# Kernel tuning notes

Hardware: AMD Instinct MI355X
Metric: run time of the kernel (lower is better)

## Reference

```python
import jax, jax.numpy as jnp
import numpy as np

B, CIN, H, W = 8, 128, 64, 64
COUT, KH, KW = 128, 3, 3
STRIDE = (1, 1)
PAD = (1, 1)
DIL = (1, 1)
GROUPS = 1
OFFSET_GROUPS = 1

def _out_size(i, k, s, p, d):
    return (i + 2 * p - d * (k - 1) - 1) // s + 1

HO = _out_size(H, KH, STRIDE[0], PAD[0], DIL[0])
WO = _out_size(W, KW, STRIDE[1], PAD[1], DIL[1])


def setup_inputs() -> dict:
    key = jax.random.key(0)
    k1, k2, k3, k4 = jax.random.split(key, 4)
    x = jax.random.normal(k1, (B, CIN, H, W), jnp.float32)
    offset = jax.random.normal(k2, (B, 2 * OFFSET_GROUPS * KH * KW, HO, WO), jnp.float32)
    fan_in = (CIN // GROUPS) * KH * KW
    bound = 1.0 / np.sqrt(fan_in)
    weight = jax.random.uniform(k3, (COUT, CIN // GROUPS, KH, KW), jnp.float32, -bound, bound)
    bias = jax.random.uniform(k4, (COUT,), jnp.float32, -bound, bound)
    return {"x": x, "offset": offset, "weight": weight, "bias": bias}


def _deform_conv2d(x, offset, weight, bias):
    Bn, Cin, Hi, Wi = x.shape
    K = KH * KW
    Goff, Gw = OFFSET_GROUPS, GROUPS
    Cpg = Cin // Goff

    # base sampling positions (before learned offsets)
    ys = jnp.arange(HO, dtype=jnp.float32) * STRIDE[0] - PAD[0]  # [HO]
    xs = jnp.arange(WO, dtype=jnp.float32) * STRIDE[1] - PAD[1]  # [WO]
    base_y = jnp.repeat(jnp.arange(KH, dtype=jnp.float32) * DIL[0], KW)  # [K]
    base_x = jnp.tile(jnp.arange(KW, dtype=jnp.float32) * DIL[1], KH)    # [K]

    # offsets: channel layout is 2*(g*K + k) + {0: dy, 1: dx}
    off = offset.reshape(Bn, Goff, K, 2, HO, WO)
    py = base_y[None, None, :, None, None] + ys[None, None, None, :, None] + off[:, :, :, 0]  # [B,Goff,K,HO,WO]
    px = base_x[None, None, :, None, None] + xs[None, None, None, None, :] + off[:, :, :, 1]

    y0 = jnp.floor(py)
    x0 = jnp.floor(px)
    ly = py - y0  # fractional weights
    lx = px - x0

    xg = x.reshape(Bn, Goff, Cpg, Hi * Wi)

    def gather_one(img, lin):  # img [Cpg, H*W], lin [K,HO,WO] -> [Cpg,K,HO,WO]
        return img[:, lin]

    gather = jax.vmap(jax.vmap(gather_one))  # over B and Goff

    def corner(yi, xi, w):
        # zero-padding semantics: out-of-bounds corner contributes 0
        mask = (yi >= 0) & (yi < Hi) & (xi >= 0) & (xi < Wi)
        iy = jnp.clip(yi, 0, Hi - 1).astype(jnp.int32)
        ix = jnp.clip(xi, 0, Wi - 1).astype(jnp.int32)
        lin = iy * Wi + ix  # [B,Goff,K,HO,WO]
        wm = (w * mask.astype(x.dtype))[:, :, None]  # broadcast over channel axis
        return gather(xg, lin) * wm  # [B,Goff,Cpg,K,HO,WO]

    val = (corner(y0, x0, (1 - ly) * (1 - lx))
           + corner(y0, x0 + 1, (1 - ly) * lx)
           + corner(y0 + 1, x0, ly * (1 - lx))
           + corner(y0 + 1, x0 + 1, ly * lx))  # [B,Goff,Cpg,K,HO,WO]

    # grouped conv accumulate
    val = val.reshape(Bn, Gw, Cin // Gw, K, HO, WO)
    wg = weight.reshape(Gw, COUT // Gw, Cin // Gw, K)
    out = jnp.einsum('bgckhw,gock->bgohw', val, wg).reshape(Bn, COUT, HO, WO)
    return out + bias[None, :, None, None]


def reference(x, offset, weight, bias):
    return _deform_conv2d(x, offset, weight, bias)
```

## Files before the change

kernel.cpp:

```cpp
#include <hip/hip_runtime.h>

typedef unsigned int   u32;
typedef unsigned short u16;
typedef short bf16x8 __attribute__((ext_vector_type(8)));
typedef float f32x4  __attribute__((ext_vector_type(4)));

#define CIN   128
#define COUT  128
#define Hh    64
#define Ww    64
#define Bb    8
#define KPOS  9
#define KDIM  (CIN*KPOS)
#define NKSTEP 36
#define XT_ELEMS (Bb*Hh*Ww*CIN)

__device__ __forceinline__ float bflo(u32 u){ return __uint_as_float(u << 16); }
__device__ __forceinline__ float bfhi(u32 u){ return __uint_as_float(u & 0xffff0000u); }

__device__ __forceinline__ u32 packbf(float a, float b){
    u32 ua = __float_as_uint(a);
    u32 ub = __float_as_uint(b);
    ua += 0x7fffu + ((ua >> 16) & 1u);
    ub += 0x7fffu + ((ub >> 16) & 1u);
    return (ua >> 16) | (ub & 0xffff0000u);
}
__device__ __forceinline__ u16 tobf(float a){
    u32 ua = __float_as_uint(a);
    ua += 0x7fffu + ((ua >> 16) & 1u);
    return (u16)(ua >> 16);
}

__global__ __launch_bounds__(256) void k_transpose(const float* __restrict__ x,
                                                   u16* __restrict__ xT){
    __shared__ float tile[32*33];
    int bi = blockIdx.x;
    int st = bi & 127, ct = (bi >> 7) & 3, b = bi >> 9;
    int sb = st * 32, cb = ct * 32;
    int tid = threadIdx.x;

    int i = tid >> 5, j = tid & 31;
    const float* xp = x + ((size_t)(b*CIN + cb) * 4096) + sb;
#pragma unroll
    for (int rr = 0; rr < 4; ++rr){
        int ci = i + rr*8;
        tile[ci*33 + j] = xp[(size_t)ci*4096 + j];
    }
    __syncthreads();

    int ii = tid >> 4, jj = tid & 15;
    u32* outp = (u32*)xT + ((size_t)b*4096 + sb)*64 + (cb >> 1) + jj;
#pragma unroll
    for (int rr = 0; rr < 2; ++rr){
        int sl = ii + rr*16;
        float v0 = tile[(2*jj  )*33 + sl];
        float v1 = tile[(2*jj+1)*33 + sl];
        outp[(size_t)sl*64] = packbf(v0, v1);
    }
}

__global__ __launch_bounds__(256) void k_wprep(const float* __restrict__ w,
                                               u16* __restrict__ Wt){
    int gid = blockIdx.x*256 + threadIdx.x;
    int jf   = gid & 7;
    int lane = (gid >> 3) & 63;
    int mt   = (gid >> 9) & 7;
    int kt   = gid >> 12;
    int m  = mt*16 + (lane & 15);
    int kk = (lane >> 4)*8 + jf;
    int ck = kt*32 + kk;
    int kpos = ck >> 7;
    int cin  = ck & 127;
    Wt[gid] = tobf(w[((size_t)m*128 + cin)*9 + kpos]);
}

__global__ __launch_bounds__(256, 2)
void k_main(const float* __restrict__ off, const float* __restrict__ bias,
            const u16* __restrict__ xT, const u16* __restrict__ Wt,
            float* __restrict__ out){
    __shared__ u32 Vsm[2][64*20];

    int tid = threadIdx.x;
    int bi  = blockIdx.x;
    int b   = bi & 7;
    int t   = bi >> 3;
    int s0  = t * 64;

    int p  = tid >> 2, qt = tid & 3;
    int ho = t;
    int wo = p;
    const u16* xb_base = xT + (size_t)b * (Hh*Ww*CIN);

    int lane = tid & 63, wave = tid >> 6;
    int wm = wave >> 1, wn = wave & 1;
    int quad = lane >> 4, l16 = lane & 15;

    f32x4 acc[4][2];
#pragma unroll
    for (int i = 0; i < 4; ++i)
#pragma unroll
        for (int j = 0; j < 2; ++j) acc[i][j] = {0.f, 0.f, 0.f, 0.f};

    int   aa[4];
    float wt[4];

    auto state = [&](int kpos){
        int kh = kpos / 3, kw = kpos - kh*3;
        size_t ob = ((size_t)(b*18 + 2*kpos))*4096 + (s0 + p);
        float dy = off[ob];
        float dx = off[ob + 4096];
        float py = (float)(ho + kh - 1) + dy;
        float px = (float)(wo + kw - 1) + dx;
        float y0f = floorf(py), x0f = floorf(px);
        float ly = py - y0f, lx = px - x0f;
        int y0 = (int)y0f, x0 = (int)x0f;
        int y1 = y0 + 1,  x1 = x0 + 1;
        float my0 = (y0 >= 0 && y0 < Hh) ? 1.f : 0.f;
        float my1 = (y1 >= 0 && y1 < Hh) ? 1.f : 0.f;
        float mx0 = (x0 >= 0 && x0 < Ww) ? 1.f : 0.f;
        float mx1 = (x1 >= 0 && x1 < Ww) ? 1.f : 0.f;
        float omly = 1.f - ly, omlx = 1.f - lx;
        wt[0] = omly*omlx*my0*mx0;
        wt[1] = omly*lx  *my0*mx1;
        wt[2] = ly  *omlx*my1*mx0;
        wt[3] = ly  *lx  *my1*mx1;
        int cy0 = min(max(y0,0),Hh-1), cy1 = min(max(y1,0),Hh-1);
        int cx0 = min(max(x0,0),Ww-1), cx1 = min(max(x1,0),Ww-1);
        aa[0] = (cy0*Ww + cx0)*CIN;
        aa[1] = (cy0*Ww + cx1)*CIN;
        aa[2] = (cy1*Ww + cx0)*CIN;
        aa[3] = (cy1*Ww + cx1)*CIN;
    };

    auto gather = [&](int ks, uint4 q[4]){
        int coff = ((ks & 3) << 5) + qt*8;
        const u16* xb = xb_base + coff;
#pragma unroll
        for (int c = 0; c < 4; ++c)
            q[c] = *(const uint4*)(xb + aa[c]);
    };

    auto loadA = [&](int ks, uint4 a[4]){
#pragma unroll
        for (int i = 0; i < 4; ++i)
            a[i] = *(const uint4*)(Wt + (size_t)(((ks*8 + wm*4 + i)*64 + lane))*8);
    };

    auto blend_store = [&](const uint4 q[4], int buf){
        u32 res[4];
#pragma unroll
        for (int d = 0; d < 4; ++d){
            float lo = 0.f, hi = 0.f;
#pragma unroll
            for (int c = 0; c < 4; ++c){
                u32 u = ((const u32*)&q[0])[c*4 + d];
                lo = fmaf(wt[c], bflo(u), lo);
                hi = fmaf(wt[c], bfhi(u), hi);
            }
            res[d] = packbf(lo, hi);
        }
        *(uint4*)&Vsm[buf][p*20 + qt*4] = *(uint4*)&res[0];
    };

    uint4 q[4], araw_cur[4], araw_nxt[4];
    state(0);
    gather(0, q);
    loadA(0, araw_cur);
    blend_store(q, 0);

    for (int ks = 0; ks < NKSTEP; ++ks){
        __syncthreads();
        int nxt = ks + 1;
        bool have_nxt = (nxt < NKSTEP);
        if (have_nxt){
            if ((nxt & 3) == 0) state(nxt >> 2);
            gather(nxt, q);
            loadA(nxt, araw_nxt);
        }

        uint4 braw[2];
#pragma unroll
        for (int j = 0; j < 2; ++j)
            braw[j] = *(const uint4*)&Vsm[ks & 1][((wn*2 + j)*16 + l16)*20 + quad*4];
#pragma unroll
        for (int i = 0; i < 4; ++i){
            bf16x8 av = __builtin_bit_cast(bf16x8, araw_cur[i]);
#pragma unroll
            for (int j = 0; j < 2; ++j){
                bf16x8 bv = __builtin_bit_cast(bf16x8, braw[j]);
                acc[i][j] = __builtin_amdgcn_mfma_f32_16x16x32_bf16(av, bv, acc[i][j], 0, 0, 0);
            }
        }

        if (have_nxt){
            blend_store(q, nxt & 1);
#pragma unroll
            for (int i = 0; i < 4; ++i) araw_cur[i] = araw_nxt[i];
        }
    }

#pragma unroll
    for (int i = 0; i < 4; ++i){
        int cout0 = (wm*4 + i)*16 + quad*4;
#pragma unroll
        for (int j = 0; j < 2; ++j){
            int pcol = (wn*2 + j)*16 + l16;
            size_t obase = ((size_t)(b*COUT + cout0))*4096 + (s0 + pcol);
#pragma unroll
            for (int r = 0; r < 4; ++r){
                out[obase + (size_t)r*4096] = acc[i][j][r] + bias[cout0 + r];
            }
        }
    }
}

extern "C" void kernel_launch(void* const* d_in, const int* in_sizes, int n_in,
                              void* d_out, int out_size, void* d_ws, size_t ws_size,
                              hipStream_t stream){
    const float* x    = (const float*)d_in[0];
    const float* off  = (const float*)d_in[1];
    const float* w    = (const float*)d_in[2];
    const float* bias = (const float*)d_in[3];
    float* out = (float*)d_out;

    u16* xT = (u16*)d_ws;
    u16* Wt = xT + XT_ELEMS;

    k_transpose<<<dim3(4096), dim3(256), 0, stream>>>(x, xT);
    k_wprep    <<<dim3(576),  dim3(256), 0, stream>>>(w, Wt);
    k_main     <<<dim3(512),  dim3(256), 0, stream>>>(off, bias, xT, Wt, out);
}
```

Before: 107.7 us.

## Gather full kernel-position channel span per stage and merge prep kernels

The main loop now processes one kernel position (all 128 channels) per stage. Each thread gathers 64 contiguous bytes per bilinear corner and blends them into a four-plane LDS buffer, so each pipeline stage runs four MFMA sub-steps under a single barrier instead of one barrier per 32-channel step. The offset load is issued before the blend so its latency is hidden. The transpose and weight-prep kernels are merged into one launch to remove a kernel launch. In exchange, the 16-register gather buffer and larger LDS footprint raise register and LDS pressure, which may reduce occupancy.

```diff
diff --git a/kernel.cpp b/kernel.cpp
--- a/kernel.cpp
+++ b/kernel.cpp
@@ -11,8 +11,8 @@
 #define Ww    64
 #define Bb    8
 #define KPOS  9
-#define KDIM  (CIN*KPOS)
-#define NKSTEP 36
+#define NSS   9
+#define PLANE 1288
 #define XT_ELEMS (Bb*Hh*Ww*CIN)
 
 __device__ __forceinline__ float bflo(u32 u){ return __uint_as_float(u << 16); }
@@ -31,54 +31,53 @@
     return (u16)(ua >> 16);
 }
 
-__global__ __launch_bounds__(256) void k_transpose(const float* __restrict__ x,
-                                                   u16* __restrict__ xT){
+__global__ __launch_bounds__(256) void k_prep(const float* __restrict__ x,
+                                              const float* __restrict__ w,
+                                              u16* __restrict__ xT,
+                                              u16* __restrict__ Wt){
     __shared__ float tile[32*33];
-    int bi = blockIdx.x;
-    int st = bi & 127, ct = (bi >> 7) & 3, b = bi >> 9;
-    int sb = st * 32, cb = ct * 32;
+    int bi  = blockIdx.x;
     int tid = threadIdx.x;
-
-    int i = tid >> 5, j = tid & 31;
-    const float* xp = x + ((size_t)(b*CIN + cb) * 4096) + sb;
-#pragma unroll
-    for (int rr = 0; rr < 4; ++rr){
-        int ci = i + rr*8;
-        tile[ci*33 + j] = xp[(size_t)ci*4096 + j];
+    if (bi < 4096){
+        int st = bi & 127, ct = (bi >> 7) & 3, b = bi >> 9;
+        int sb = st * 32, cb = ct * 32;
+        int i = tid >> 5, j = tid & 31;
+        const float* xp = x + ((size_t)(b*CIN + cb) * 4096) + sb;
+#pragma unroll
+        for (int rr = 0; rr < 4; ++rr){
+            int ci = i + rr*8;
+            tile[ci*33 + j] = xp[(size_t)ci*4096 + j];
+        }
+        __syncthreads();
+        int ii = tid >> 4, jj = tid & 15;
+        u32* outp = (u32*)xT + ((size_t)b*4096 + sb)*64 + (cb >> 1) + jj;
+#pragma unroll
+        for (int rr = 0; rr < 2; ++rr){
+            int sl = ii + rr*16;
+            float v0 = tile[(2*jj  )*33 + sl];
+            float v1 = tile[(2*jj+1)*33 + sl];
+            outp[(size_t)sl*64] = packbf(v0, v1);
+        }
+    } else {
+        int gid = (bi - 4096)*256 + tid;
+        int jf   = gid & 7;
+        int lane = (gid >> 3) & 63;
+        int mt   = (gid >> 9) & 7;
+        int kt   = gid >> 12;
+        int m  = mt*16 + (lane & 15);
+        int kk = (lane >> 4)*8 + jf;
+        int ck = kt*32 + kk;
+        int kpos = ck >> 7;
+        int cin  = ck & 127;
+        Wt[gid] = tobf(w[((size_t)m*128 + cin)*9 + kpos]);
     }
-    __syncthreads();
-
-    int ii = tid >> 4, jj = tid & 15;
-    u32* outp = (u32*)xT + ((size_t)b*4096 + sb)*64 + (cb >> 1) + jj;
-#pragma unroll
-    for (int rr = 0; rr < 2; ++rr){
-        int sl = ii + rr*16;
-        float v0 = tile[(2*jj  )*33 + sl];
-        float v1 = tile[(2*jj+1)*33 + sl];
-        outp[(size_t)sl*64] = packbf(v0, v1);
-    }
-}
-
-__global__ __launch_bounds__(256) void k_wprep(const float* __restrict__ w,
-                                               u16* __restrict__ Wt){
-    int gid = blockIdx.x*256 + threadIdx.x;
-    int jf   = gid & 7;
-    int lane = (gid >> 3) & 63;
-    int mt   = (gid >> 9) & 7;
-    int kt   = gid >> 12;
-    int m  = mt*16 + (lane & 15);
-    int kk = (lane >> 4)*8 + jf;
-    int ck = kt*32 + kk;
-    int kpos = ck >> 7;
-    int cin  = ck & 127;
-    Wt[gid] = tobf(w[((size_t)m*128 + cin)*9 + kpos]);
 }
 
 __global__ __launch_bounds__(256, 2)
 void k_main(const float* __restrict__ off, const float* __restrict__ bias,
             const u16* __restrict__ xT, const u16* __restrict__ Wt,
             float* __restrict__ out){
-    __shared__ u32 Vsm[2][64*20];
+    __shared__ u32 Vsm[2][4*PLANE];
 
     int tid = threadIdx.x;
     int bi  = blockIdx.x;
@@ -89,7 +88,7 @@
     int p  = tid >> 2, qt = tid & 3;
     int ho = t;
     int wo = p;
-    const u16* xb_base = xT + (size_t)b * (Hh*Ww*CIN);
+    const u16* xb_base = xT + (size_t)b * (Hh*Ww*CIN) + qt*32;
 
     int lane = tid & 63, wave = tid >> 6;
     int wm = wave >> 1, wn = wave & 1;
@@ -103,14 +102,19 @@
 
     int   aa[4];
     float wt[4];
-
-    auto state = [&](int kpos){
+    float dyr, dxr;
+    uint4 q[16];
+    uint4 araw[2][4];
+
+    auto off_load = [&](int kpos){
+        size_t ob = ((size_t)(b*18 + 2*kpos))*4096 + (s0 + p);
+        dyr = off[ob];
+        dxr = off[ob + 4096];
+    };
+    auto state_calc = [&](int kpos){
         int kh = kpos / 3, kw = kpos - kh*3;
-        size_t ob = ((size_t)(b*18 + 2*kpos))*4096 + (s0 + p);
-        float dy = off[ob];
-        float dx = off[ob + 4096];
-        float py = (float)(ho + kh - 1) + dy;
-        float px = (float)(wo + kw - 1) + dx;
+        float py = (float)(ho + kh - 1) + dyr;
+        float px = (float)(wo + kw - 1) + dxr;
         float y0f = floorf(py), x0f = floorf(px);
         float ly = py - y0f, lx = px - x0f;
         int y0 = (int)y0f, x0 = (int)x0f;
@@ -131,71 +135,72 @@
         aa[2] = (cy1*Ww + cx0)*CIN;
         aa[3] = (cy1*Ww + cx1)*CIN;
     };
-
-    auto gather = [&](int ks, uint4 q[4]){
-        int coff = ((ks & 3) << 5) + qt*8;
-        const u16* xb = xb_base + coff;
-#pragma unroll
-        for (int c = 0; c < 4; ++c)
-            q[c] = *(const uint4*)(xb + aa[c]);
-    };
-
+    auto gather = [&](){
+#pragma unroll
+        for (int c = 0; c < 4; ++c){
+            const u16* s = xb_base + aa[c];
+#pragma unroll
+            for (int u = 0; u < 4; ++u)
+                q[c*4 + u] = *(const uint4*)(s + u*8);
+        }
+    };
+    auto blend_store = [&](int buf){
+        u32* dst = &Vsm[buf][qt*PLANE + p*20];
+#pragma unroll
+        for (int u = 0; u < 4; ++u){
+            u32 res[4];
+#pragma unroll
+            for (int d = 0; d < 4; ++d){
+                float lo = 0.f, hi = 0.f;
+#pragma unroll
+                for (int c = 0; c < 4; ++c){
+                    u32 v = ((const u32*)&q[c*4 + u])[d];
+                    lo = fmaf(wt[c], bflo(v), lo);
+                    hi = fmaf(wt[c], bfhi(v), hi);
+                }
+                res[d] = packbf(lo, hi);
+            }
+            *(uint4*)(dst + u*4) = *(const uint4*)res;
+        }
+    };
     auto loadA = [&](int ks, uint4 a[4]){
 #pragma unroll
         for (int i = 0; i < 4; ++i)
             a[i] = *(const uint4*)(Wt + (size_t)(((ks*8 + wm*4 + i)*64 + lane))*8);
     };
 
-    auto blend_store = [&](const uint4 q[4], int buf){
-        u32 res[4];
-#pragma unroll
-        for (int d = 0; d < 4; ++d){
-            float lo = 0.f, hi = 0.f;
-#pragma unroll
-            for (int c = 0; c < 4; ++c){
-                u32 u = ((const u32*)&q[0])[c*4 + d];
-                lo = fmaf(wt[c], bflo(u), lo);
-                hi = fmaf(wt[c], bfhi(u), hi);
+    off_load(0);
+    state_calc(0);
+    gather();
+    loadA(0, araw[0]);
+
+    for (int kp = 0; kp < NSS; ++kp){
+        bool have_nxt = (kp + 1 < NSS);
+        if (have_nxt) off_load(kp + 1);
+        blend_store(kp & 1);
+        if (have_nxt){
+            state_calc(kp + 1);
+            gather();
+        }
+        __syncthreads();
+
+#pragma unroll
+        for (int ks2 = 0; ks2 < 4; ++ks2){
+            int flat = kp*4 + ks2;
+            if (flat < 35) loadA(flat + 1, araw[(ks2+1) & 1]);
+            uint4 braw[2];
+#pragma unroll
+            for (int j = 0; j < 2; ++j)
+                braw[j] = *(const uint4*)&Vsm[kp & 1][ks2*PLANE + ((wn*2 + j)*16 + l16)*20 + quad*4];
+#pragma unroll
+            for (int i = 0; i < 4; ++i){
+                bf16x8 av = __builtin_bit_cast(bf16x8, araw[ks2 & 1][i]);
+#pragma unroll
+                for (int j = 0; j < 2; ++j){
+                    bf16x8 bv = __builtin_bit_cast(bf16x8, braw[j]);
+                    acc[i][j] = __builtin_amdgcn_mfma_f32_16x16x32_bf16(av, bv, acc[i][j], 0, 0, 0);
+                }
             }
-            res[d] = packbf(lo, hi);
-        }
-        *(uint4*)&Vsm[buf][p*20 + qt*4] = *(uint4*)&res[0];
-    };
-
-    uint4 q[4], araw_cur[4], araw_nxt[4];
-    state(0);
-    gather(0, q);
-    loadA(0, araw_cur);
-    blend_store(q, 0);
-
-    for (int ks = 0; ks < NKSTEP; ++ks){
-        __syncthreads();
-        int nxt = ks + 1;
-        bool have_nxt = (nxt < NKSTEP);
-        if (have_nxt){
-            if ((nxt & 3) == 0) state(nxt >> 2);
-            gather(nxt, q);
-            loadA(nxt, araw_nxt);
-        }
-
-        uint4 braw[2];
-#pragma unroll
-        for (int j = 0; j < 2; ++j)
-            braw[j] = *(const uint4*)&Vsm[ks & 1][((wn*2 + j)*16 + l16)*20 + quad*4];
-#pragma unroll
-        for (int i = 0; i < 4; ++i){
-            bf16x8 av = __builtin_bit_cast(bf16x8, araw_cur[i]);
-#pragma unroll
-            for (int j = 0; j < 2; ++j){
-                bf16x8 bv = __builtin_bit_cast(bf16x8, braw[j]);
-                acc[i][j] = __builtin_amdgcn_mfma_f32_16x16x32_bf16(av, bv, acc[i][j], 0, 0, 0);
-            }
-        }
-
-        if (have_nxt){
-            blend_store(q, nxt & 1);
-#pragma unroll
-            for (int i = 0; i < 4; ++i) araw_cur[i] = araw_nxt[i];
         }
     }
 
@@ -226,7 +231,6 @@
     u16* xT = (u16*)d_ws;
     u16* Wt = xT + XT_ELEMS;
 
-    k_transpose<<<dim3(4096), dim3(256), 0, stream>>>(x, xT);
-    k_wprep    <<<dim3(576),  dim3(256), 0, stream>>>(w, Wt);
-    k_main     <<<dim3(512),  dim3(256), 0, stream>>>(off, bias, xT, Wt, out);
-}
+    k_prep<<<dim3(4672), dim3(256), 0, stream>>>(x, w, xT, Wt);
+    k_main<<<dim3(512),  dim3(256), 0, stream>>>(off, bias, xT, Wt, out);
+}
```

After: 107.8 us. Within noise of the previous version (+0.1%).
